# Kernel optimization log

Hardware: AMD Instinct MI355X
Metric: run time of the kernel (lower is better)

The kernel has to match this reference:

```python
import jax, jax.numpy as jnp
import numpy as np

LN_EPS = 1e-5


def setup_inputs() -> dict:
    key = jax.random.key(0)
    k_h, k_s, k_d, k_w = jax.random.split(key, 4)
    N, E, F_IN, F_OUT = 100000, 1600000, 128, 128
    h = jax.random.normal(k_h, (N, F_IN), dtype=jnp.float32)
    src = jax.random.randint(k_s, (E,), 0, N, dtype=jnp.int32)
    dst = jax.random.randint(k_d, (E,), 0, N, dtype=jnp.int32)
    # Linear(2*in_feats, out_feats): weight [out, 2*in], bias [out]
    W = jax.random.normal(k_w, (F_OUT, 2 * F_IN), dtype=jnp.float32) * (1.0 / np.sqrt(2 * F_IN))
    b = jnp.zeros((F_OUT,), dtype=jnp.float32)
    gamma = jnp.ones((F_OUT,), dtype=jnp.float32)
    beta = jnp.zeros((F_OUT,), dtype=jnp.float32)
    return {"h": h, "src": src, "dst": dst, "W": W, "b": b, "gamma": gamma, "beta": beta}


def reference(h, src, dst, W, b, gamma, beta):
    N = h.shape[0]
    # mean aggregation: update_all(copy_src('h','m'), mean('m','h'))
    msg_sum = jax.ops.segment_sum(h[src], dst, num_segments=N)          # [N, F]
    deg = jax.ops.segment_sum(jnp.ones_like(dst, dtype=h.dtype), dst, num_segments=N)  # [N]
    ah = msg_sum / jnp.maximum(deg, 1.0)[:, None]                        # zero-degree -> 0 (DGL mean gives 0)
    # concat + linear
    hc = jnp.concatenate([h, ah], axis=1)                                # [N, 2F]
    z = hc @ W.T + b                                                     # [N, out]
    # LayerNorm (elementwise affine)
    mu = jnp.mean(z, axis=-1, keepdims=True)
    var = jnp.mean((z - mu) ** 2, axis=-1, keepdims=True)
    z = (z - mu) * jax.lax.rsqrt(var + LN_EPS) * gamma + beta
    # activation = relu
    return jax.nn.relu(z)
```

## Files before the change

kernel.cpp:

```cpp
#include <hip/hip_runtime.h>
#include <stdint.h>

#define FDIM 128
#define NBITS 6
#define BNODES 64
#define CAP 1536
#define PBATCH 8192

typedef __attribute__((ext_vector_type(8))) short bf16x8;
typedef __attribute__((ext_vector_type(4))) float f32x4;
typedef __attribute__((ext_vector_type(8))) unsigned short u16x8;

__device__ __forceinline__ unsigned short f32_to_bf16(float f) {
  union { float f; uint32_t u; } v; v.f = f;
  uint32_t u = v.u;
  u += 0x7FFFu + ((u >> 16) & 1u);
  return (unsigned short)(u >> 16);
}
__device__ __forceinline__ float bf16_to_f32(unsigned short h) {
  union { uint32_t u; float f; } v; v.u = ((uint32_t)h) << 16;
  return v.f;
}

__device__ __forceinline__ void gload_lds16(const void* g, void* l) {
  __builtin_amdgcn_global_load_lds(
      (const __attribute__((address_space(1))) void*)g,
      (__attribute__((address_space(3))) void*)l, 16, 0, 0);
}

__global__ void cvt_bf16_8(const float* __restrict__ in, unsigned short* __restrict__ o, int n8) {
  int i = blockIdx.x * blockDim.x + threadIdx.x;
  if (i >= n8) return;
  float4 a = ((const float4*)in)[i * 2], b = ((const float4*)in)[i * 2 + 1];
  u16x8 r;
  r[0] = f32_to_bf16(a.x); r[1] = f32_to_bf16(a.y); r[2] = f32_to_bf16(a.z); r[3] = f32_to_bf16(a.w);
  r[4] = f32_to_bf16(b.x); r[5] = f32_to_bf16(b.y); r[6] = f32_to_bf16(b.z); r[7] = f32_to_bf16(b.w);
  ((u16x8*)o)[i] = r;
}

__global__ __launch_bounds__(256) void partition_edges(
    const int* __restrict__ src, const int* __restrict__ dst,
    int* __restrict__ gcur, unsigned int* __restrict__ pairs, int E, int nbk) {
  __shared__ int hist[1600];
  for (int k = threadIdx.x; k < nbk; k += 256) hist[k] = 0;
  __syncthreads();
  int base = blockIdx.x * PBATCH;
  const int4* d4p = (const int4*)(dst + base);
  const int4* s4p = (const int4*)(src + base);
#pragma unroll
  for (int j = 0; j < PBATCH / 1024; ++j) {
    int vi = j * 256 + threadIdx.x;
    int i0 = base + vi * 4;
    if (i0 < E) {
      int4 d = d4p[vi];
      atomicAdd(&hist[d.x >> NBITS], 1);
      if (i0 + 1 < E) atomicAdd(&hist[d.y >> NBITS], 1);
      if (i0 + 2 < E) atomicAdd(&hist[d.z >> NBITS], 1);
      if (i0 + 3 < E) atomicAdd(&hist[d.w >> NBITS], 1);
    }
  }
  __syncthreads();
  for (int k = threadIdx.x; k < nbk; k += 256) {
    int c = hist[k];
    hist[k] = (c > 0) ? atomicAdd(&gcur[k], c) : 0;
  }
  __syncthreads();
#pragma unroll
  for (int j = 0; j < PBATCH / 1024; ++j) {
    int vi = j * 256 + threadIdx.x;
    int i0 = base + vi * 4;
    if (i0 < E) {
      int4 d = d4p[vi];
      int4 s = s4p[vi];
#pragma unroll
      for (int q = 0; q < 4; ++q) {
        if (i0 + q >= E) break;
        int dd = (q == 0) ? d.x : (q == 1) ? d.y : (q == 2) ? d.z : d.w;
        int ss = (q == 0) ? s.x : (q == 1) ? s.y : (q == 2) ? s.z : s.w;
        int b = dd >> NBITS;
        int pos = atomicAdd(&hist[b], 1);
        if (pos < CAP)
          pairs[(size_t)b * CAP + pos] = ((unsigned)ss << NBITS) | (unsigned)(dd & (BNODES - 1));
      }
    }
  }
}

__global__ __launch_bounds__(256) void sort_aggregate(
    const unsigned short* __restrict__ h2, const int* __restrict__ gcur,
    const unsigned int* __restrict__ pairs, unsigned short* __restrict__ ah2, int N) {
  __shared__ int cnt[BNODES];
  __shared__ int off[BNODES];
  __shared__ int cur[BNODES];
  __shared__ int lsrc[CAP];
  int b = blockIdx.x >> 1;
  int half = blockIdx.x & 1;
  int n0 = b << NBITS;
  int tid = threadIdx.x;
  int ec = gcur[b]; if (ec > CAP) ec = CAP;
  if (tid < BNODES) cnt[tid] = 0;
  __syncthreads();
  const unsigned int* pb = pairs + (size_t)b * CAP;
  for (int e = tid; e < ec; e += 256) atomicAdd(&cnt[pb[e] & (BNODES - 1)], 1);
  __syncthreads();
  if (tid < BNODES) off[tid] = cnt[tid];
  __syncthreads();
  for (int s = 1; s < BNODES; s <<= 1) {
    int v = 0;
    if (tid < BNODES && tid >= s) v = off[tid - s];
    __syncthreads();
    if (tid < BNODES) off[tid] += v;
    __syncthreads();
  }
  if (tid < BNODES) { int e0 = off[tid] - cnt[tid]; off[tid] = e0; cur[tid] = e0; }
  __syncthreads();
  for (int e = tid; e < ec; e += 256) {
    unsigned int p = pb[e];
    int pos = atomicAdd(&cur[p & (BNODES - 1)], 1);
    lsrc[pos] = (int)(p >> NBITS);
  }
  __syncthreads();
  int g = tid >> 4, lane = tid & 15;
  for (int ln = half * 32 + g; ln < half * 32 + 32; ln += 16) {
    int node = n0 + ln;
    if (node >= N) break;
    int s0 = off[ln], d = cnt[ln];
    int e = s0, eend = s0 + d;
    float a0[8] = {0,0,0,0,0,0,0,0}, a1[8] = {0,0,0,0,0,0,0,0};
    float a2[8] = {0,0,0,0,0,0,0,0}, a3[8] = {0,0,0,0,0,0,0,0};
    for (; e + 4 <= eend; e += 4) {
      u16x8 v0 = *(const u16x8*)(h2 + (size_t)lsrc[e]     * 128 + lane * 8);
      u16x8 v1 = *(const u16x8*)(h2 + (size_t)lsrc[e + 1] * 128 + lane * 8);
      u16x8 v2 = *(const u16x8*)(h2 + (size_t)lsrc[e + 2] * 128 + lane * 8);
      u16x8 v3 = *(const u16x8*)(h2 + (size_t)lsrc[e + 3] * 128 + lane * 8);
#pragma unroll
      for (int j = 0; j < 8; ++j) {
        a0[j] += bf16_to_f32(v0[j]); a1[j] += bf16_to_f32(v1[j]);
        a2[j] += bf16_to_f32(v2[j]); a3[j] += bf16_to_f32(v3[j]);
      }
    }
    for (; e < eend; ++e) {
      u16x8 v = *(const u16x8*)(h2 + (size_t)lsrc[e] * 128 + lane * 8);
#pragma unroll
      for (int j = 0; j < 8; ++j) a0[j] += bf16_to_f32(v[j]);
    }
    float inv = 1.0f / (float)(d > 0 ? d : 1);
    u16x8 r;
#pragma unroll
    for (int j = 0; j < 8; ++j)
      r[j] = f32_to_bf16(((a0[j] + a1[j]) + (a2[j] + a3[j])) * inv);
    *(u16x8*)(ah2 + (size_t)node * 128 + lane * 8) = r;
  }
}

__global__ __launch_bounds__(256) void gemm_mfma_ln_relu(
    const unsigned short* __restrict__ h2, const unsigned short* __restrict__ ah2,
    const unsigned short* __restrict__ W2, const float* __restrict__ bias,
    const float* __restrict__ gamma, const float* __restrict__ beta,
    float* __restrict__ out, int N) {
  __shared__ unsigned short As[128 * 64];
  __shared__ unsigned short Ws[128 * 64];
  int tid = threadIdx.x;
  int w = tid >> 6, l = tid & 63;
  int lr = l & 15, lg = l >> 4;
  int n0 = blockIdx.x * 128;

  f32x4 acc[2][8];
#pragma unroll
  for (int rt = 0; rt < 2; ++rt)
#pragma unroll
    for (int ct = 0; ct < 8; ++ct) acc[rt][ct] = (f32x4){0.f, 0.f, 0.f, 0.f};

  for (int kt = 0; kt < 4; ++kt) {
    const unsigned short* abase = (kt < 2) ? h2 : ah2;
#pragma unroll
    for (int rd = 0; rd < 4; ++rd) {
      int off = rd * 4096 + tid * 16;
      int r = off >> 7;
      int s = (off >> 4) & 7;
      int ls = s ^ (r & 7);
      int gn = n0 + r; if (gn > N - 1) gn = N - 1;
      gload_lds16((const char*)abase + (size_t)gn * 256 + (size_t)(kt & 1) * 128 + ls * 16,
                  (char*)As + off);
      gload_lds16((const char*)W2 + (size_t)r * 512 + (size_t)kt * 128 + ls * 16,
                  (char*)Ws + off);
    }
    __syncthreads();

    bf16x8 aF[2][2], bF[8][2];
#pragma unroll
    for (int rt = 0; rt < 2; ++rt)
#pragma unroll
      for (int kc = 0; kc < 2; ++kc) {
        int r = w * 32 + rt * 16 + lr;
        int slot = kc * 4 + lg;
        aF[rt][kc] = *(const bf16x8*)((const char*)As + r * 128 + ((slot ^ (r & 7)) * 16));
      }
#pragma unroll
    for (int ct = 0; ct < 8; ++ct)
#pragma unroll
      for (int kc = 0; kc < 2; ++kc) {
        int r = ct * 16 + lr;
        int slot = kc * 4 + lg;
        bF[ct][kc] = *(const bf16x8*)((const char*)Ws + r * 128 + ((slot ^ (r & 7)) * 16));
      }
#pragma unroll
    for (int rt = 0; rt < 2; ++rt)
#pragma unroll
      for (int ct = 0; ct < 8; ++ct)
#pragma unroll
        for (int kc = 0; kc < 2; ++kc)
          acc[rt][ct] = __builtin_amdgcn_mfma_f32_16x16x32_bf16(
              aF[rt][kc], bF[ct][kc], acc[rt][ct], 0, 0, 0);
    __syncthreads();
  }

  float bj[8], gj[8], tj[8];
#pragma unroll
  for (int ct = 0; ct < 8; ++ct) {
    int c = ct * 16 + lr;
    bj[ct] = bias[c]; gj[ct] = gamma[c]; tj[ct] = beta[c];
  }
#pragma unroll
  for (int rt = 0; rt < 2; ++rt)
#pragma unroll
    for (int q = 0; q < 4; ++q) {
      int n = n0 + w * 32 + rt * 16 + lg * 4 + q;
      float v[8], s = 0.f, s2 = 0.f;
#pragma unroll
      for (int ct = 0; ct < 8; ++ct) {
        v[ct] = acc[rt][ct][q] + bj[ct];
        s += v[ct]; s2 += v[ct] * v[ct];
      }
#pragma unroll
      for (int off = 1; off < 16; off <<= 1) {
        s  += __shfl_xor(s, off);
        s2 += __shfl_xor(s2, off);
      }
      float mean = s * (1.f / 128.f);
      float var = s2 * (1.f / 128.f) - mean * mean;
      float rstd = rsqrtf(var + 1e-5f);
      if (n < N) {
#pragma unroll
        for (int ct = 0; ct < 8; ++ct) {
          float o = (v[ct] - mean) * rstd * gj[ct] + tj[ct];
          out[(size_t)n * FDIM + ct * 16 + lr] = fmaxf(o, 0.f);
        }
      }
    }
}

extern "C" void kernel_launch(void* const* d_in, const int* in_sizes, int n_in,
                              void* d_out, int out_size, void* d_ws, size_t ws_size,
                              hipStream_t stream) {
  const float* h     = (const float*)d_in[0];
  const int*   src   = (const int*)d_in[1];
  const int*   dst   = (const int*)d_in[2];
  const float* W     = (const float*)d_in[3];
  const float* bias  = (const float*)d_in[4];
  const float* gamma = (const float*)d_in[5];
  const float* beta  = (const float*)d_in[6];
  float* out = (float*)d_out;
  int N = in_sizes[0] / FDIM;
  int E = in_sizes[1];
  int nbk = (N + BNODES - 1) >> NBITS;

  int* gcur = (int*)d_ws;
  unsigned int* pairs = (unsigned int*)((char*)d_ws + 8192);
  unsigned short* h2  = (unsigned short*)((char*)pairs + (size_t)nbk * CAP * 4);
  unsigned short* ah2 = h2 + (size_t)N * 128;
  unsigned short* W2  = ah2 + (size_t)N * 128;

  hipMemsetAsync(gcur, 0, (size_t)nbk * 4, stream);
  cvt_bf16_8<<<(N * FDIM / 8 + 255) / 256, 256, 0, stream>>>(h, h2, N * FDIM / 8);
  cvt_bf16_8<<<(FDIM * 2 * FDIM / 8 + 255) / 256, 256, 0, stream>>>(W, W2, FDIM * 2 * FDIM / 8);
  partition_edges<<<(E + PBATCH - 1) / PBATCH, 256, 0, stream>>>(src, dst, gcur, pairs, E, nbk);
  sort_aggregate<<<nbk * 2, 256, 0, stream>>>(h2, gcur, pairs, ah2, N);
  gemm_mfma_ln_relu<<<(N + 127) / 128, 256, 0, stream>>>(h2, ah2, W2, bias, gamma, beta, out, N);
}
```

Baseline: 225.4 us.

## Split bucket sort and neighbor gather into separate kernels with finer node parallelism

The fused sort+aggregate kernel, which redid the bucket sort in two half-blocks, is replaced by two kernels. The first sorts each bucket once and writes sorted source ids back to global memory along with per-node offsets and degrees. The second gathers with one 16-lane group per node across many small blocks, unrolling eight loads deep for more memory-level parallelism and using cheaper bf16 unpacking. This removes the duplicated sort work and the LDS-limited occupancy of the old kernel, at the cost of an extra launch and a global round trip for the sorted ids.

Result: slower. 234.4 us (+4.0%).

```diff
diff --git a/kernel.cpp b/kernel.cpp
--- a/kernel.cpp
+++ b/kernel.cpp
@@ -17,9 +17,11 @@
   u += 0x7FFFu + ((u >> 16) & 1u);
   return (unsigned short)(u >> 16);
 }
-__device__ __forceinline__ float bf16_to_f32(unsigned short h) {
-  union { uint32_t u; float f; } v; v.u = ((uint32_t)h) << 16;
-  return v.f;
+__device__ __forceinline__ float u32lo_bf16(uint32_t u) {
+  union { uint32_t u; float f; } v; v.u = u << 16; return v.f;
+}
+__device__ __forceinline__ float u32hi_bf16(uint32_t u) {
+  union { uint32_t u; float f; } v; v.u = u & 0xFFFF0000u; return v.f;
 }
 
 __device__ __forceinline__ void gload_lds16(const void* g, void* l) {
@@ -86,22 +88,23 @@
   }
 }
 
-__global__ __launch_bounds__(256) void sort_aggregate(
-    const unsigned short* __restrict__ h2, const int* __restrict__ gcur,
-    const unsigned int* __restrict__ pairs, unsigned short* __restrict__ ah2, int N) {
+__global__ __launch_bounds__(256) void fine_sort(
+    const int* __restrict__ gcur, unsigned int* __restrict__ pairs,
+    int* __restrict__ noff, int* __restrict__ ndeg, int N) {
+  __shared__ int larr[CAP];
+  __shared__ int sorted_[CAP];
   __shared__ int cnt[BNODES];
   __shared__ int off[BNODES];
   __shared__ int cur[BNODES];
-  __shared__ int lsrc[CAP];
-  int b = blockIdx.x >> 1;
-  int half = blockIdx.x & 1;
+  int b = blockIdx.x;
   int n0 = b << NBITS;
   int tid = threadIdx.x;
   int ec = gcur[b]; if (ec > CAP) ec = CAP;
   if (tid < BNODES) cnt[tid] = 0;
-  __syncthreads();
-  const unsigned int* pb = pairs + (size_t)b * CAP;
-  for (int e = tid; e < ec; e += 256) atomicAdd(&cnt[pb[e] & (BNODES - 1)], 1);
+  unsigned int* pb = pairs + (size_t)b * CAP;
+  for (int e = tid; e < ec; e += 256) larr[e] = (int)pb[e];
+  __syncthreads();
+  for (int e = tid; e < ec; e += 256) atomicAdd(&cnt[larr[e] & (BNODES - 1)], 1);
   __syncthreads();
   if (tid < BNODES) off[tid] = cnt[tid];
   __syncthreads();
@@ -115,42 +118,68 @@
   if (tid < BNODES) { int e0 = off[tid] - cnt[tid]; off[tid] = e0; cur[tid] = e0; }
   __syncthreads();
   for (int e = tid; e < ec; e += 256) {
-    unsigned int p = pb[e];
+    int p = larr[e];
     int pos = atomicAdd(&cur[p & (BNODES - 1)], 1);
-    lsrc[pos] = (int)(p >> NBITS);
-  }
-  __syncthreads();
-  int g = tid >> 4, lane = tid & 15;
-  for (int ln = half * 32 + g; ln < half * 32 + 32; ln += 16) {
-    int node = n0 + ln;
-    if (node >= N) break;
-    int s0 = off[ln], d = cnt[ln];
-    int e = s0, eend = s0 + d;
-    float a0[8] = {0,0,0,0,0,0,0,0}, a1[8] = {0,0,0,0,0,0,0,0};
-    float a2[8] = {0,0,0,0,0,0,0,0}, a3[8] = {0,0,0,0,0,0,0,0};
-    for (; e + 4 <= eend; e += 4) {
-      u16x8 v0 = *(const u16x8*)(h2 + (size_t)lsrc[e]     * 128 + lane * 8);
-      u16x8 v1 = *(const u16x8*)(h2 + (size_t)lsrc[e + 1] * 128 + lane * 8);
-      u16x8 v2 = *(const u16x8*)(h2 + (size_t)lsrc[e + 2] * 128 + lane * 8);
-      u16x8 v3 = *(const u16x8*)(h2 + (size_t)lsrc[e + 3] * 128 + lane * 8);
-#pragma unroll
-      for (int j = 0; j < 8; ++j) {
-        a0[j] += bf16_to_f32(v0[j]); a1[j] += bf16_to_f32(v1[j]);
-        a2[j] += bf16_to_f32(v2[j]); a3[j] += bf16_to_f32(v3[j]);
-      }
-    }
-    for (; e < eend; ++e) {
-      u16x8 v = *(const u16x8*)(h2 + (size_t)lsrc[e] * 128 + lane * 8);
-#pragma unroll
-      for (int j = 0; j < 8; ++j) a0[j] += bf16_to_f32(v[j]);
-    }
-    float inv = 1.0f / (float)(d > 0 ? d : 1);
-    u16x8 r;
-#pragma unroll
-    for (int j = 0; j < 8; ++j)
-      r[j] = f32_to_bf16(((a0[j] + a1[j]) + (a2[j] + a3[j])) * inv);
-    *(u16x8*)(ah2 + (size_t)node * 128 + lane * 8) = r;
-  }
+    sorted_[pos] = p >> NBITS;
+  }
+  __syncthreads();
+  for (int e = tid; e < ec; e += 256) pb[e] = (unsigned int)sorted_[e];
+  if (tid < BNODES) {
+    int node = n0 + tid;
+    if (node < N) { noff[node] = b * CAP + off[tid]; ndeg[node] = cnt[tid]; }
+  }
+}
+
+__global__ __launch_bounds__(256) void gather_mean(
+    const unsigned short* __restrict__ h2, const int* __restrict__ noff,
+    const int* __restrict__ ndeg, const unsigned int* __restrict__ ssrc,
+    unsigned short* __restrict__ ah2, int N) {
+  int node = blockIdx.x * 16 + (threadIdx.x >> 4);
+  int lane = threadIdx.x & 15;
+  if (node >= N) return;
+  int o = noff[node], d = ndeg[node];
+  const uint4* h4 = (const uint4*)h2;
+  float l0[4] = {0,0,0,0}, h0[4] = {0,0,0,0}, l1[4] = {0,0,0,0}, h1[4] = {0,0,0,0};
+  float l2[4] = {0,0,0,0}, h2a[4] = {0,0,0,0}, l3[4] = {0,0,0,0}, h3[4] = {0,0,0,0};
+  int e = 0;
+  for (; e + 8 <= d; e += 8) {
+    int s0 = ssrc[o + e],     s1 = ssrc[o + e + 1], s2 = ssrc[o + e + 2], s3 = ssrc[o + e + 3];
+    int s4 = ssrc[o + e + 4], s5 = ssrc[o + e + 5], s6 = ssrc[o + e + 6], s7 = ssrc[o + e + 7];
+    uint4 v0 = h4[(size_t)s0 * 16 + lane], v1 = h4[(size_t)s1 * 16 + lane];
+    uint4 v2 = h4[(size_t)s2 * 16 + lane], v3 = h4[(size_t)s3 * 16 + lane];
+    uint4 v4 = h4[(size_t)s4 * 16 + lane], v5 = h4[(size_t)s5 * 16 + lane];
+    uint4 v6 = h4[(size_t)s6 * 16 + lane], v7 = h4[(size_t)s7 * 16 + lane];
+    uint32_t u;
+#define ACC(vv, LL, HH)                                              \
+    u = vv.x; LL[0] += u32lo_bf16(u); HH[0] += u32hi_bf16(u);        \
+    u = vv.y; LL[1] += u32lo_bf16(u); HH[1] += u32hi_bf16(u);        \
+    u = vv.z; LL[2] += u32lo_bf16(u); HH[2] += u32hi_bf16(u);        \
+    u = vv.w; LL[3] += u32lo_bf16(u); HH[3] += u32hi_bf16(u);
+    ACC(v0, l0, h0) ACC(v1, l1, h1) ACC(v2, l2, h2a) ACC(v3, l3, h3)
+    ACC(v4, l0, h0) ACC(v5, l1, h1) ACC(v6, l2, h2a) ACC(v7, l3, h3)
+  }
+  for (; e + 4 <= d; e += 4) {
+    int s0 = ssrc[o + e], s1 = ssrc[o + e + 1], s2 = ssrc[o + e + 2], s3 = ssrc[o + e + 3];
+    uint4 v0 = h4[(size_t)s0 * 16 + lane], v1 = h4[(size_t)s1 * 16 + lane];
+    uint4 v2 = h4[(size_t)s2 * 16 + lane], v3 = h4[(size_t)s3 * 16 + lane];
+    uint32_t u;
+    ACC(v0, l0, h0) ACC(v1, l1, h1) ACC(v2, l2, h2a) ACC(v3, l3, h3)
+  }
+  for (; e < d; ++e) {
+    int s0 = ssrc[o + e];
+    uint4 v0 = h4[(size_t)s0 * 16 + lane];
+    uint32_t u;
+    ACC(v0, l0, h0)
+#undef ACC
+  }
+  float inv = 1.0f / (float)(d > 0 ? d : 1);
+  u16x8 r;
+#pragma unroll
+  for (int q = 0; q < 4; ++q) {
+    r[2 * q]     = f32_to_bf16(((l0[q] + l1[q]) + (l2[q] + l3[q])) * inv);
+    r[2 * q + 1] = f32_to_bf16(((h0[q] + h1[q]) + (h2a[q] + h3[q])) * inv);
+  }
+  *(u16x8*)(ah2 + (size_t)node * 128 + lane * 8) = r;
 }
 
 __global__ __launch_bounds__(256) void gemm_mfma_ln_relu(
@@ -266,7 +295,9 @@
   int nbk = (N + BNODES - 1) >> NBITS;
 
   int* gcur = (int*)d_ws;
-  unsigned int* pairs = (unsigned int*)((char*)d_ws + 8192);
+  int* noff = (int*)((char*)d_ws + 8192);
+  int* ndeg = noff + ((N + 63) / 64) * 64;
+  unsigned int* pairs = (unsigned int*)(ndeg + ((N + 63) / 64) * 64);
   unsigned short* h2  = (unsigned short*)((char*)pairs + (size_t)nbk * CAP * 4);
   unsigned short* ah2 = h2 + (size_t)N * 128;
   unsigned short* W2  = ah2 + (size_t)N * 128;
@@ -275,6 +306,7 @@
   cvt_bf16_8<<<(N * FDIM / 8 + 255) / 256, 256, 0, stream>>>(h, h2, N * FDIM / 8);
   cvt_bf16_8<<<(FDIM * 2 * FDIM / 8 + 255) / 256, 256, 0, stream>>>(W, W2, FDIM * 2 * FDIM / 8);
   partition_edges<<<(E + PBATCH - 1) / PBATCH, 256, 0, stream>>>(src, dst, gcur, pairs, E, nbk);
-  sort_aggregate<<<nbk * 2, 256, 0, stream>>>(h2, gcur, pairs, ah2, N);
+  fine_sort<<<nbk, 256, 0, stream>>>(gcur, pairs, noff, ndeg, N);
+  gather_mean<<<(N + 15) / 16, 256, 0, stream>>>(h2, noff, ndeg, pairs, ah2, N);
   gemm_mfma_ln_relu<<<(N + 127) / 128, 256, 0, stream>>>(h2, ah2, W2, bias, gamma, beta, out, N);
 }
```
